# Optimization experiments

Hardware: AMD Instinct MI355X
Metric: run time of the kernel (lower is better)

## Reference

```python
import jax, jax.numpy as jnp
import numpy as np

D = 512      # model_size
NH = 8       # num_heads
HD = D // NH # head_dim = 64
T = 2048     # seq len (qlen == klen == pos len)
B = 2        # batch

# flattened Bayesian parameter layout (matches flatten_list order in the module)
_SHAPES = [(3 * D, D), (D, D), (D, D), (3 * D,), (D,), (D,), (NH, HD), (NH, HD)]
_N = sum(int(np.prod(s)) for s in _SHAPES)  # 1,314,304


def _unflatten(w):
    out, i = [], 0
    for s in _SHAPES:
        n = int(np.prod(s))
        out.append(w[i:i + n].reshape(s))
        i += n
    return out


def _rel_shift(x):
    # Transformer-XL relative shift: x is [qlen, klen, B, NH]
    q, k, b, n = x.shape
    x = jnp.pad(x, ((0, 0), (1, 0), (0, 0), (0, 0)))  # zero col at front of klen axis
    x = x.reshape(k + 1, q, b, n)[1:]
    return x.reshape(q, k, b, n)


def setup_inputs() -> dict:
    key = jax.random.key(0)
    k1, k2, k3, k4, k5 = jax.random.split(key, 5)
    inp = jax.random.normal(k1, (T, B, D), dtype=jnp.float32)
    pos = jax.random.normal(k2, (T, 1, D), dtype=jnp.float32)
    std = np.sqrt(2.0 / (D + D))
    mu = jax.random.normal(k3, (_N,), dtype=jnp.float32) * std
    rho = -5.0 + 0.1 * jax.random.normal(k4, (_N,), dtype=jnp.float32)
    eps = jax.random.normal(k5, (_N,), dtype=jnp.float32)
    attn_mask = jnp.triu(jnp.ones((T, T), dtype=bool), 1)  # True = masked (future)
    return {"input": inp, "pos": pos, "attn_mask": attn_mask,
            "mu": mu, "rho": rho, "eps": eps}


def reference(input, pos, attn_mask, mu, rho, eps):
    # Gaussian reparameterized weight sample: w = mu + softplus(rho) * eps
    w = mu + jax.nn.softplus(rho) * eps
    (in_w, out_w, pos_w, in_b, out_b, pos_b, r_w_bias, r_r_bias) = _unflatten(w)

    # input projection -> q, k, v : [T, B, NH, HD]
    qkv = input @ in_w.T + in_b                      # [T, B, 3D]
    q, k, v = jnp.split(qkv, 3, axis=-1)
    q = q.reshape(T, B, NH, HD)
    k = k.reshape(T, B, NH, HD)
    v = v.reshape(T, B, NH, HD)

    # relative position projection: [R, NH, HD]
    r = (pos[:, 0, :] @ pos_w.T + pos_b).reshape(-1, NH, HD)

    # content score (AC) and position score (BD) with rel-shift
    AC = jnp.einsum('ibnd,jbnd->ijbn', q + r_w_bias, k)
    BD = _rel_shift(jnp.einsum('ibnd,jnd->ijbn', q + r_r_bias, r))

    scale = np.float32(1.0 / np.sqrt(HD))
    score = (AC + BD) * scale                        # [T, T, B, NH]
    score = jnp.where(attn_mask[:, :, None, None],
                      jnp.finfo(score.dtype).min, score)
    probs = jax.nn.softmax(score, axis=1)

    attn_vec = jnp.einsum('ijbn,jbnd->ibnd', probs, v).reshape(T, B, D)
    return attn_vec @ out_w.T + out_b                # [T, B, D]
```

## Files before the change

kernel.cpp:

```cpp
#include <hip/hip_runtime.h>


typedef float f32x4 __attribute__((ext_vector_type(4)));
typedef short bf16x8 __attribute__((ext_vector_type(8)));

#define NW 1314304
#define OFF_INB  1310720
#define OFF_INW  0
#define OFF_OUTW 786432
#define OFF_POSW 1048576
#define BB_IN  0
#define BB_OUT 1536
#define BB_POS 2048
#define BB_RW  2560
#define BB_RR  3072

#define L2E 1.44269504088896340736f

__device__ __forceinline__ unsigned short f2bf(float x) {
  unsigned u = __builtin_bit_cast(unsigned, x);
  u += 0x7fffu + ((u >> 16) & 1u);
  return (unsigned short)(u >> 16);
}
__device__ __forceinline__ unsigned pk2(float lo, float hi) {
  return (unsigned)f2bf(lo) | ((unsigned)f2bf(hi) << 16);
}

__global__ void prep_kernel(const float* __restrict__ mu, const float* __restrict__ rho,
                            const float* __restrict__ eps,
                            const float* __restrict__ input, const float* __restrict__ pos,
                            unsigned short* __restrict__ Wh, float* __restrict__ Bf,
                            unsigned short* __restrict__ inH, unsigned short* __restrict__ posH) {
  const int bx = blockIdx.x;
  if (bx < 1284) {
    int i = (bx * 256 + threadIdx.x) * 4;
    if (i < NW) {
      float4 m = *(const float4*)&mu[i];
      float4 r = *(const float4*)&rho[i];
      float4 e = *(const float4*)&eps[i];
      float w0 = m.x + ((r.x > 20.f) ? r.x : log1pf(expf(r.x))) * e.x;
      float w1 = m.y + ((r.y > 20.f) ? r.y : log1pf(expf(r.y))) * e.y;
      float w2 = m.z + ((r.z > 20.f) ? r.z : log1pf(expf(r.z))) * e.z;
      float w3 = m.w + ((r.w > 20.f) ? r.w : log1pf(expf(r.w))) * e.w;
      union { unsigned short s[4]; uint2 u; } p;
      p.s[0] = f2bf(w0); p.s[1] = f2bf(w1); p.s[2] = f2bf(w2); p.s[3] = f2bf(w3);
      *(uint2*)&Wh[i] = p.u;
      if (i >= OFF_INB) {
        float4 b; b.x = w0; b.y = w1; b.z = w2; b.w = w3;
        *(float4*)&Bf[i - OFF_INB] = b;
      }
    }
  } else if (bx < 3332) {
    int i = ((bx - 1284) * 256 + threadIdx.x) * 4;
    float4 v = *(const float4*)&input[i];
    union { unsigned short s[4]; uint2 u; } p;
    p.s[0] = f2bf(v.x); p.s[1] = f2bf(v.y); p.s[2] = f2bf(v.z); p.s[3] = f2bf(v.w);
    *(uint2*)&inH[i] = p.u;
  } else {
    int i = ((bx - 3332) * 256 + threadIdx.x) * 4;
    float4 v = *(const float4*)&pos[i];
    union { unsigned short s[4]; uint2 u; } p;
    p.s[0] = f2bf(v.x); p.s[1] = f2bf(v.y); p.s[2] = f2bf(v.z); p.s[3] = f2bf(v.w);
    *(uint2*)&posH[i] = p.u;
  }
}

__device__ __forceinline__ void gemm_loop(const unsigned short* __restrict__ A,
                                          const unsigned short* __restrict__ B,
                                          unsigned short* As, unsigned short* Bs,
                                          f32x4 (&acc)[4]) {
  const int tid = threadIdx.x;
  const int wv = tid >> 6, lane = tid & 63, g = lane >> 4, cc = lane & 15;
  const int row = tid >> 2, q4 = tid & 3;
  const unsigned short* Ap = A + (size_t)row * 512 + 16 * q4;
  const unsigned short* Bp = B + (size_t)row * 512 + 16 * q4;

  *(uint4*)&As[row * 72 + 16 * q4]     = *(const uint4*)Ap;
  *(uint4*)&As[row * 72 + 16 * q4 + 8] = *(const uint4*)(Ap + 8);
  *(uint4*)&Bs[row * 72 + 16 * q4]     = *(const uint4*)Bp;
  *(uint4*)&Bs[row * 72 + 16 * q4 + 8] = *(const uint4*)(Bp + 8);
  __syncthreads();

  for (int it = 0; it < 8; it++) {
    uint4 a0, a1, b0, b1;
    const bool pf = (it < 7);
    if (pf) {
      const unsigned short* An = Ap + 64 * (it + 1);
      const unsigned short* Bn = Bp + 64 * (it + 1);
      a0 = *(const uint4*)An; a1 = *(const uint4*)(An + 8);
      b0 = *(const uint4*)Bn; b1 = *(const uint4*)(Bn + 8);
    }
    __builtin_amdgcn_s_setprio(1);
#pragma unroll
    for (int ks = 0; ks < 2; ks++) {
      bf16x8 af = *(const bf16x8*)&As[(16 * wv + cc) * 72 + 32 * ks + 8 * g];
#pragma unroll
      for (int fn = 0; fn < 4; fn++) {
        bf16x8 bf = *(const bf16x8*)&Bs[(16 * fn + cc) * 72 + 32 * ks + 8 * g];
        acc[fn] = __builtin_amdgcn_mfma_f32_16x16x32_bf16(af, bf, acc[fn], 0, 0, 0);
      }
    }
    __builtin_amdgcn_s_setprio(0);
    __syncthreads();
    if (pf) {
      *(uint4*)&As[row * 72 + 16 * q4]     = a0;
      *(uint4*)&As[row * 72 + 16 * q4 + 8] = a1;
      *(uint4*)&Bs[row * 72 + 16 * q4]     = b0;
      *(uint4*)&Bs[row * 72 + 16 * q4 + 8] = b1;
    }
    __syncthreads();
  }
}

__global__ __launch_bounds__(256, 2)
void gemm01_kernel(const unsigned short* __restrict__ inH, const unsigned short* __restrict__ posH,
                   const unsigned short* __restrict__ Wh, const float* __restrict__ Bf,
                   unsigned short* __restrict__ qrw, unsigned short* __restrict__ qrr,
                   unsigned short* __restrict__ kbuf, unsigned short* __restrict__ vT,
                   unsigned short* __restrict__ rbuf) {
  __shared__ __align__(16) unsigned short As[64 * 72];
  __shared__ __align__(16) unsigned short Bs[64 * 72];
  const int bx = blockIdx.x;
  const int tid = threadIdx.x;
  const int wv = tid >> 6, lane = tid & 63, g = lane >> 4, cc = lane & 15;

  const bool isR = (bx >= 1536);
  int m0, n0;
  const unsigned short *A, *W;
  if (!isR) {
    m0 = (bx & 63) << 6; n0 = (bx >> 6) << 6;
    A = inH + (size_t)m0 * 512;  W = Wh + OFF_INW + (size_t)n0 * 512;
  } else {
    const int t = bx - 1536;
    m0 = (t & 31) << 6; n0 = (t >> 5) << 6;
    A = posH + (size_t)m0 * 512; W = Wh + OFF_POSW + (size_t)n0 * 512;
  }

  f32x4 acc[4];
#pragma unroll
  for (int i = 0; i < 4; i++) { acc[i][0] = 0.f; acc[i][1] = 0.f; acc[i][2] = 0.f; acc[i][3] = 0.f; }
  gemm_loop(A, W, As, Bs, acc);

#pragma unroll
  for (int fn = 0; fn < 4; fn++) {
    const int col = n0 + 16 * fn + cc;
#pragma unroll
    for (int r = 0; r < 4; r++) {
      const int mrow = m0 + 16 * wv + 4 * g + r;
      float v = acc[fn][r];
      if (!isR) {
        v += Bf[BB_IN + col];
        const int sec = col >> 9;
        const int d = col & 511;
        const int nh = d >> 6, hd = d & 63;
        const int t = mrow >> 1, bb = mrow & 1;
        const size_t bi = ((size_t)(bb * 8 + nh) * 2048 + t) * 64 + hd;
        if (sec == 0) {
          qrw[bi] = f2bf(v + Bf[BB_RW + d]);
          qrr[bi] = f2bf(v + Bf[BB_RR + d]);
        } else if (sec == 1) {
          kbuf[bi] = f2bf(v);
        } else {
          vT[((size_t)(bb * 8 + nh) * 64 + hd) * 2048 + t] = f2bf(v);
        }
      } else {
        v += Bf[BB_POS + col];
        rbuf[((size_t)(col >> 6) * 2048 + mrow) * 64 + (col & 63)] = f2bf(v);
      }
    }
  }
}

__global__ __launch_bounds__(256, 2)
void gemmO_kernel(const unsigned short* __restrict__ av, const unsigned short* __restrict__ W,
                  const float* __restrict__ Bf, float* __restrict__ outp) {
  __shared__ __align__(16) unsigned short As[64 * 72];
  __shared__ __align__(16) unsigned short Bs[64 * 72];
  const int bx = blockIdx.x;
  const int tid = threadIdx.x;
  const int wv = tid >> 6, lane = tid & 63, g = lane >> 4, cc = lane & 15;
  const int m0 = (bx & 63) << 6, n0 = (bx >> 6) << 6;

  f32x4 acc[4];
#pragma unroll
  for (int i = 0; i < 4; i++) { acc[i][0] = 0.f; acc[i][1] = 0.f; acc[i][2] = 0.f; acc[i][3] = 0.f; }
  gemm_loop(av + (size_t)m0 * 512, W + (size_t)n0 * 512, As, Bs, acc);

#pragma unroll
  for (int fn = 0; fn < 4; fn++) {
    const int col = n0 + 16 * fn + cc;
#pragma unroll
    for (int r = 0; r < 4; r++) {
      const int mrow = m0 + 16 * wv + 4 * g + r;
      outp[(size_t)mrow * 512 + col] = acc[fn][r] + Bf[BB_OUT + col];
    }
  }
}

__global__ __launch_bounds__(256, 2)
void attn_kernel(const unsigned short* __restrict__ qrw, const unsigned short* __restrict__ qrr,
                 const unsigned short* __restrict__ kb, const unsigned short* __restrict__ vt,
                 const unsigned short* __restrict__ rb, unsigned short* __restrict__ av)
{
  __shared__ __align__(16) unsigned short Ks[64 * 72];
  __shared__ __align__(16) unsigned short Vs[64 * 72];
  __shared__ __align__(16) unsigned short Rs[128 * 72];
  __shared__ __align__(16) float Gs[4 * 80 * 20];

  const int tid = threadIdx.x;
  const int wv = tid >> 6, lane = tid & 63, g = lane >> 4, cc = lane & 15;
  const int bx = (int)blockIdx.x;
  const int idx = bx & 255;
  const int qt = (bx >> 8) ? (idx >> 4) : (31 - (idx >> 4));
  const int bn = idx & 15;
  const int nh = bn & 7, bb = bn >> 3;
  const int i0 = qt * 64;
  const int i0g = i0 + wv * 16;
  const int w0base = 1984 - i0;

  const size_t qko = (size_t)bn * 2048 * 64;
  const size_t ro = (size_t)nh * 2048 * 64;

  bf16x8 qw[2], qr[2];
#pragma unroll
  for (int ks = 0; ks < 2; ks++) {
    qw[ks] = *(const bf16x8*)&qrw[qko + (size_t)(i0g + cc) * 64 + 32 * ks + 8 * g];
    qr[ks] = *(const bf16x8*)&qrr[qko + (size_t)(i0g + cc) * 64 + 32 * ks + 8 * g];
  }

  float m_run = -3.0e38f, l_run = 0.f;
  f32x4 o[4];
#pragma unroll
  for (int i = 0; i < 4; i++) { o[i][0] = 0.f; o[i][1] = 0.f; o[i][2] = 0.f; o[i][3] = 0.f; }

  const int srow = tid >> 2, sq = tid & 3;
  const int rrow = tid >> 1, rhalf = tid & 1;
  float* Gw = &Gs[wv * 1600];
  const int rbase = 48 - 16 * wv;

  {
    const unsigned short* kp = &kb[qko + (size_t)srow * 64 + 16 * sq];
    *(uint4*)&Ks[srow * 72 + 16 * sq]     = *(const uint4*)kp;
    *(uint4*)&Ks[srow * 72 + 16 * sq + 8] = *(const uint4*)(kp + 8);
    const unsigned short* vp = &vt[qko + (size_t)srow * 2048 + 16 * sq];
    *(uint4*)&Vs[srow * 72 + 16 * sq]     = *(const uint4*)vp;
    *(uint4*)&Vs[srow * 72 + 16 * sq + 8] = *(const uint4*)(vp + 8);
    const int u0 = w0base + rrow;
    const int uc0 = u0 > 2047 ? 2047 : u0;
    const unsigned short* rp = &rb[ro + (size_t)uc0 * 64 + 32 * rhalf];
    unsigned short* rd = &Rs[(u0 & 127) * 72 + 32 * rhalf];
    *(uint4*)rd        = *(const uint4*)rp;
    *(uint4*)(rd + 8)  = *(const uint4*)(rp + 8);
    *(uint4*)(rd + 16) = *(const uint4*)(rp + 16);
    *(uint4*)(rd + 24) = *(const uint4*)(rp + 24);
  }
  __syncthreads();

  for (int kt = 0; kt <= qt; kt++) {
    const int j0 = kt * 64;
    const int w0k = w0base + j0;
    const bool pf = (kt < qt);

    uint4 ka0, ka1, va0, va1, ra0, ra1;
    int rslot = 0;
    if (pf) {
      const unsigned short* kp = &kb[qko + (size_t)(j0 + 64 + srow) * 64 + 16 * sq];
      ka0 = *(const uint4*)kp; ka1 = *(const uint4*)(kp + 8);
      const unsigned short* vp = &vt[qko + (size_t)srow * 2048 + j0 + 64 + 16 * sq];
      va0 = *(const uint4*)vp; va1 = *(const uint4*)(vp + 8);
      const int unew = w0k + 128 + (tid >> 2);
      rslot = unew & 127;
      const int uc = unew > 2047 ? 2047 : unew;
      const unsigned short* rp = &rb[ro + (size_t)uc * 64 + 16 * sq];
      ra0 = *(const uint4*)rp; ra1 = *(const uint4*)(rp + 8);
    }

    f32x4 st[4];
#pragma unroll
    for (int i = 0; i < 4; i++) { st[i][0] = 0.f; st[i][1] = 0.f; st[i][2] = 0.f; st[i][3] = 0.f; }
    __builtin_amdgcn_s_setprio(1);
#pragma unroll
    for (int ks = 0; ks < 2; ks++) {
#pragma unroll
      for (int fm = 0; fm < 4; fm++) {
        bf16x8 ka = *(const bf16x8*)&Ks[(16 * fm + cc) * 72 + 32 * ks + 8 * g];
        st[fm] = __builtin_amdgcn_mfma_f32_16x16x32_bf16(ka, qw[ks], st[fm], 0, 0, 0);
      }
    }
    f32x4 gt[5];
#pragma unroll
    for (int i = 0; i < 5; i++) { gt[i][0] = 0.f; gt[i][1] = 0.f; gt[i][2] = 0.f; gt[i][3] = 0.f; }
    const int rr0 = w0k + rbase + cc;
#pragma unroll
    for (int ks = 0; ks < 2; ks++) {
#pragma unroll
      for (int fm = 0; fm < 5; fm++) {
        const int rrw = (rr0 + 16 * fm) & 127;
        bf16x8 ra = *(const bf16x8*)&Rs[rrw * 72 + 32 * ks + 8 * g];
        gt[fm] = __builtin_amdgcn_mfma_f32_16x16x32_bf16(ra, qr[ks], gt[fm], 0, 0, 0);
      }
    }
    __builtin_amdgcn_s_setprio(0);
#pragma unroll
    for (int fm = 0; fm < 5; fm++)
#pragma unroll
      for (int r = 0; r < 4; r++)
        Gw[(16 * fm + 4 * g + r) * 20 + cc] = gt[fm][r];

    float p[4][4];
    float tm = -3.0e38f;
    const bool diag = (kt == qt);
#pragma unroll
    for (int fm = 0; fm < 4; fm++) {
#pragma unroll
      for (int r = 0; r < 4; r++) {
        const int jj = 16 * fm + 4 * g + r;
        float bd = Gw[(jj - cc + 15) * 20 + cc];
        float sv = (st[fm][r] + bd) * 0.125f;
        if (diag && (jj > cc + 16 * wv)) sv = -3.0e38f;
        p[fm][r] = sv;
        tm = fmaxf(tm, sv);
      }
    }
    tm = fmaxf(tm, __shfl_xor(tm, 16));
    tm = fmaxf(tm, __shfl_xor(tm, 32));
    const float m_new = fmaxf(m_run, tm);
    const float sc = exp2f((m_run - m_new) * L2E);
    float ps = 0.f;
#pragma unroll
    for (int fm = 0; fm < 4; fm++)
#pragma unroll
      for (int r = 0; r < 4; r++) {
        float pv = exp2f((p[fm][r] - m_new) * L2E);
        p[fm][r] = pv;
        ps += pv;
      }
    ps += __shfl_xor(ps, 16);
    ps += __shfl_xor(ps, 32);
    l_run = l_run * sc + ps;
    m_run = m_new;

    float scr[4];
#pragma unroll
    for (int r = 0; r < 4; r++) scr[r] = __shfl(sc, 4 * g + r);
#pragma unroll
    for (int fn = 0; fn < 4; fn++)
#pragma unroll
      for (int r = 0; r < 4; r++) o[fn][r] *= scr[r];

    unsigned u01[4], u23[4];
#pragma unroll
    for (int fm = 0; fm < 4; fm++) {
      u01[fm] = pk2(p[fm][0], p[fm][1]);
      u23[fm] = pk2(p[fm][2], p[fm][3]);
    }
    bf16x8 pa[2];
#pragma unroll
    for (int ks = 0; ks < 2; ks++) {
      union { unsigned u[4]; bf16x8 v; } pw;
#pragma unroll
      for (int j = 0; j < 4; j++) {
        const int srcl = (2 * (g & 1) + (j >> 1)) * 16 + cc;
        unsigned v0 = __shfl((j & 1) ? u23[2 * ks] : u01[2 * ks], srcl);
        unsigned v1 = __shfl((j & 1) ? u23[2 * ks + 1] : u01[2 * ks + 1], srcl);
        pw.u[j] = (g >> 1) ? v1 : v0;
      }
      pa[ks] = pw.v;
    }
    __builtin_amdgcn_s_setprio(1);
#pragma unroll
    for (int ks = 0; ks < 2; ks++) {
#pragma unroll
      for (int fn = 0; fn < 4; fn++) {
        bf16x8 vb = *(const bf16x8*)&Vs[(16 * fn + cc) * 72 + 32 * ks + 8 * g];
        o[fn] = __builtin_amdgcn_mfma_f32_16x16x32_bf16(pa[ks], vb, o[fn], 0, 0, 0);
      }
    }
    __builtin_amdgcn_s_setprio(0);

    __syncthreads();
    if (pf) {
      *(uint4*)&Ks[srow * 72 + 16 * sq]     = ka0;
      *(uint4*)&Ks[srow * 72 + 16 * sq + 8] = ka1;
      *(uint4*)&Vs[srow * 72 + 16 * sq]     = va0;
      *(uint4*)&Vs[srow * 72 + 16 * sq + 8] = va1;
      unsigned short* rd = &Rs[rslot * 72 + 16 * sq];
      *(uint4*)rd       = ra0;
      *(uint4*)(rd + 8) = ra1;
    }
    __syncthreads();
  }

  const float inv = 1.0f / l_run;
  float invr[4];
#pragma unroll
  for (int r = 0; r < 4; r++) invr[r] = __shfl(inv, 4 * g + r);
#pragma unroll
  for (int fn = 0; fn < 4; fn++) {
    const int hd = 16 * fn + cc;
#pragma unroll
    for (int r = 0; r < 4; r++) {
      const int irow = i0g + 4 * g + r;
      av[((size_t)(irow * 2 + bb) * 8 + nh) * 64 + hd] = f2bf(o[fn][r] * invr[r]);
    }
  }
}

extern "C" void kernel_launch(void* const* d_in, const int* in_sizes, int n_in,
                              void* d_out, int out_size, void* d_ws, size_t ws_size,
                              hipStream_t stream) {
  const float* input = (const float*)d_in[0];
  const float* pos   = (const float*)d_in[1];
  const float* mu  = (const float*)d_in[3];
  const float* rho = (const float*)d_in[4];
  const float* eps = (const float*)d_in[5];
  float* out = (float*)d_out;

  char* ws = (char*)d_ws;
  unsigned short* Wh   = (unsigned short*)ws;
  float*          Bf   = (float*)(ws + 2628608);
  unsigned short* inH  = (unsigned short*)(ws + 2642944);
  unsigned short* posH = (unsigned short*)(ws + 6837248);
  unsigned short* qrw  = (unsigned short*)(ws + 8934400);
  unsigned short* qrr  = (unsigned short*)(ws + 13128704);
  unsigned short* kbuf = (unsigned short*)(ws + 17323008);
  unsigned short* vT   = (unsigned short*)(ws + 21517312);
  unsigned short* rbuf = (unsigned short*)(ws + 25711616);
  unsigned short* av   = inH;

  prep_kernel<<<dim3(4356), dim3(256), 0, stream>>>(mu, rho, eps, input, pos, Wh, Bf, inH, posH);
  gemm01_kernel<<<dim3(1792), dim3(256), 0, stream>>>(inH, posH, Wh, Bf, qrw, qrr, kbuf, vT, rbuf);
  attn_kernel<<<dim3(512), dim3(256), 0, stream>>>(qrw, qrr, kbuf, vT, rbuf, av);
  gemmO_kernel<<<dim3(512), dim3(256), 0, stream>>>(av, Wh + OFF_OUTW, Bf, out);
}
```

Baseline: 173.9 us.

## Split causal attention over key chunks with a combine pass; coalesce vT stores

The attention kernel now splits each query tile's key range into chunks of up to 8 key tiles, giving 1280 roughly balanced blocks instead of 512 with uneven causal work. Partial outputs and softmax stats are written to a workspace and merged by a new combine kernel. Separately, the V-section of the QKV GEMM transposes through shared memory so vT is written with 16-byte coalesced stores. The BD scratch buffer is stored as bf16 to cut LDS, and occupancy is raised to 3 blocks per SIMD, at the cost of an extra launch, partial-output traffic and some precision loss.

```diff
diff --git a/kernel.cpp b/kernel.cpp
--- a/kernel.cpp
+++ b/kernel.cpp
@@ -21,6 +21,9 @@
   unsigned u = __builtin_bit_cast(unsigned, x);
   u += 0x7fffu + ((u >> 16) & 1u);
   return (unsigned short)(u >> 16);
+}
+__device__ __forceinline__ float bf2f(unsigned short s) {
+  return __builtin_bit_cast(float, ((unsigned)s) << 16);
 }
 __device__ __forceinline__ unsigned pk2(float lo, float hi) {
   return (unsigned)f2bf(lo) | ((unsigned)f2bf(hi) << 16);
@@ -141,6 +144,30 @@
   for (int i = 0; i < 4; i++) { acc[i][0] = 0.f; acc[i][1] = 0.f; acc[i][2] = 0.f; acc[i][3] = 0.f; }
   gemm_loop(A, W, As, Bs, acc);
 
+  const int sec = n0 >> 9;
+  if (!isR && sec == 2) {
+#pragma unroll
+    for (int fn = 0; fn < 4; fn++) {
+      const int col = n0 + 16 * fn + cc;
+#pragma unroll
+      for (int r = 0; r < 4; r++)
+        As[(16 * wv + 4 * g + r) * 72 + 16 * fn + cc] = f2bf(acc[fn][r] + Bf[BB_IN + col]);
+    }
+    __syncthreads();
+    const int nh2 = (n0 >> 6) & 7;
+#pragma unroll
+    for (int cpass = 0; cpass < 2; cpass++) {
+      const int ch = tid + cpass * 256;
+      const int ncol = ch >> 3, bb2 = (ch >> 2) & 1, jc = ch & 3;
+      union { unsigned short s[8]; uint4 u; } pk;
+#pragma unroll
+      for (int jj = 0; jj < 8; jj++)
+        pk.s[jj] = As[(2 * (8 * jc + jj) + bb2) * 72 + ncol];
+      *(uint4*)&vT[((size_t)(bb2 * 8 + nh2) * 64 + ncol) * 2048 + (m0 >> 1) + 8 * jc] = pk.u;
+    }
+    return;
+  }
+
 #pragma unroll
   for (int fn = 0; fn < 4; fn++) {
     const int col = n0 + 16 * fn + cc;
@@ -150,7 +177,6 @@
       float v = acc[fn][r];
       if (!isR) {
         v += Bf[BB_IN + col];
-        const int sec = col >> 9;
         const int d = col & 511;
         const int nh = d >> 6, hd = d & 63;
         const int t = mrow >> 1, bb = mrow & 1;
@@ -158,10 +184,8 @@
         if (sec == 0) {
           qrw[bi] = f2bf(v + Bf[BB_RW + d]);
           qrr[bi] = f2bf(v + Bf[BB_RR + d]);
-        } else if (sec == 1) {
+        } else {
           kbuf[bi] = f2bf(v);
-        } else {
-          vT[((size_t)(bb * 8 + nh) * 64 + hd) * 2048 + t] = f2bf(v);
         }
       } else {
         v += Bf[BB_POS + col];
@@ -197,22 +221,30 @@
   }
 }
 
-__global__ __launch_bounds__(256, 2)
+__global__ __launch_bounds__(256, 3)
 void attn_kernel(const unsigned short* __restrict__ qrw, const unsigned short* __restrict__ qrr,
                  const unsigned short* __restrict__ kb, const unsigned short* __restrict__ vt,
-                 const unsigned short* __restrict__ rb, unsigned short* __restrict__ av)
+                 const unsigned short* __restrict__ rb, unsigned short* __restrict__ av,
+                 unsigned short* __restrict__ pO, float* __restrict__ pStats)
 {
   __shared__ __align__(16) unsigned short Ks[64 * 72];
   __shared__ __align__(16) unsigned short Vs[64 * 72];
   __shared__ __align__(16) unsigned short Rs[128 * 72];
-  __shared__ __align__(16) float Gs[4 * 80 * 20];
+  __shared__ __align__(16) unsigned short Gs[4 * 80 * 20];
 
   const int tid = threadIdx.x;
   const int wv = tid >> 6, lane = tid & 63, g = lane >> 4, cc = lane & 15;
   const int bx = (int)blockIdx.x;
-  const int idx = bx & 255;
-  const int qt = (bx >> 8) ? (idx >> 4) : (31 - (idx >> 4));
-  const int bn = idx & 15;
+  const int bn = bx & 15;
+  const int sid = 79 - (bx >> 4);
+  int qt, s, ns;
+  if (sid < 8)       { qt = sid;                s = 0;           ns = 1; }
+  else if (sid < 24) { qt = 8 + ((sid - 8) >> 1); s = (sid - 8) & 1; ns = 2; }
+  else if (sid < 48) { const int t = sid - 24; const int q3 = t / 3; qt = 16 + q3; s = t - 3 * q3; ns = 3; }
+  else               { const int t = sid - 48; qt = 24 + (t >> 2); s = t & 3; ns = 4; }
+  const int kt0 = s * 8;
+  const int kt1 = (kt0 + 8 < qt + 1) ? (kt0 + 8) : (qt + 1);
+
   const int nh = bn & 7, bb = bn >> 3;
   const int i0 = qt * 64;
   const int i0g = i0 + wv * 16;
@@ -235,17 +267,17 @@
 
   const int srow = tid >> 2, sq = tid & 3;
   const int rrow = tid >> 1, rhalf = tid & 1;
-  float* Gw = &Gs[wv * 1600];
+  unsigned short* Gw = &Gs[wv * 1600];
   const int rbase = 48 - 16 * wv;
 
   {
-    const unsigned short* kp = &kb[qko + (size_t)srow * 64 + 16 * sq];
+    const unsigned short* kp = &kb[qko + (size_t)(kt0 * 64 + srow) * 64 + 16 * sq];
     *(uint4*)&Ks[srow * 72 + 16 * sq]     = *(const uint4*)kp;
     *(uint4*)&Ks[srow * 72 + 16 * sq + 8] = *(const uint4*)(kp + 8);
-    const unsigned short* vp = &vt[qko + (size_t)srow * 2048 + 16 * sq];
+    const unsigned short* vp = &vt[qko + (size_t)srow * 2048 + kt0 * 64 + 16 * sq];
     *(uint4*)&Vs[srow * 72 + 16 * sq]     = *(const uint4*)vp;
     *(uint4*)&Vs[srow * 72 + 16 * sq + 8] = *(const uint4*)(vp + 8);
-    const int u0 = w0base + rrow;
+    const int u0 = w0base + kt0 * 64 + rrow;
     const int uc0 = u0 > 2047 ? 2047 : u0;
     const unsigned short* rp = &rb[ro + (size_t)uc0 * 64 + 32 * rhalf];
     unsigned short* rd = &Rs[(u0 & 127) * 72 + 32 * rhalf];
@@ -256,10 +288,10 @@
   }
   __syncthreads();
 
-  for (int kt = 0; kt <= qt; kt++) {
+  for (int kt = kt0; kt < kt1; kt++) {
     const int j0 = kt * 64;
     const int w0k = w0base + j0;
-    const bool pf = (kt < qt);
+    const bool pf = (kt + 1 < kt1);
 
     uint4 ka0, ka1, va0, va1, ra0, ra1;
     int rslot = 0;
@@ -305,7 +337,7 @@
     for (int fm = 0; fm < 5; fm++)
 #pragma unroll
       for (int r = 0; r < 4; r++)
-        Gw[(16 * fm + 4 * g + r) * 20 + cc] = gt[fm][r];
+        Gw[(16 * fm + 4 * g + r) * 20 + cc] = f2bf(gt[fm][r]);
 
     float p[4][4];
     float tm = -3.0e38f;
@@ -315,7 +347,7 @@
 #pragma unroll
       for (int r = 0; r < 4; r++) {
         const int jj = 16 * fm + 4 * g + r;
-        float bd = Gw[(jj - cc + 15) * 20 + cc];
+        float bd = bf2f(Gw[(jj - cc + 15) * 20 + cc]);
         float sv = (st[fm][r] + bd) * 0.125f;
         if (diag && (jj > cc + 16 * wv)) sv = -3.0e38f;
         p[fm][r] = sv;
@@ -391,19 +423,82 @@
     __syncthreads();
   }
 
-  const float inv = 1.0f / l_run;
-  float invr[4];
-#pragma unroll
-  for (int r = 0; r < 4; r++) invr[r] = __shfl(inv, 4 * g + r);
-#pragma unroll
-  for (int fn = 0; fn < 4; fn++) {
-    const int hd = 16 * fn + cc;
-#pragma unroll
-    for (int r = 0; r < 4; r++) {
-      const int irow = i0g + 4 * g + r;
-      av[((size_t)(irow * 2 + bb) * 8 + nh) * 64 + hd] = f2bf(o[fn][r] * invr[r]);
-    }
-  }
+  if (ns == 1) {
+    const float inv = 1.0f / l_run;
+    float invr[4];
+#pragma unroll
+    for (int r = 0; r < 4; r++) invr[r] = __shfl(inv, 4 * g + r);
+#pragma unroll
+    for (int fn = 0; fn < 4; fn++) {
+      const int hd = 16 * fn + cc;
+#pragma unroll
+      for (int r = 0; r < 4; r++) {
+        const int irow = i0g + 4 * g + r;
+        av[((size_t)(irow * 2 + bb) * 8 + nh) * 64 + hd] = f2bf(o[fn][r] * invr[r]);
+      }
+    }
+  } else {
+    const size_t slot = (size_t)(bn * 80 + sid);
+#pragma unroll
+    for (int fn = 0; fn < 4; fn++) {
+      const int hd = 16 * fn + cc;
+#pragma unroll
+      for (int r = 0; r < 4; r++)
+        pO[slot * 4096 + (16 * wv + 4 * g + r) * 64 + hd] = f2bf(o[fn][r]);
+    }
+    if (g == 0) {
+      pStats[slot * 128 + (16 * wv + cc) * 2]     = m_run;
+      pStats[slot * 128 + (16 * wv + cc) * 2 + 1] = l_run;
+    }
+  }
+}
+
+__global__ __launch_bounds__(256)
+void combine_kernel(const unsigned short* __restrict__ pO, const float* __restrict__ pStats,
+                    unsigned short* __restrict__ av) {
+  const int bxx = (int)blockIdx.x;
+  const int bn = bxx & 15, qt = 8 + (bxx >> 4);
+  const int nh = bn & 7, bb = bn >> 3;
+  const int ns = (qt >> 3) + 1;
+  const int sid0 = (qt < 16) ? (8 + (qt - 8) * 2)
+                 : (qt < 24) ? (24 + (qt - 16) * 3)
+                             : (48 + (qt - 24) * 4);
+  const int tid = threadIdx.x;
+  const int ql = tid >> 2, hq = tid & 3;
+  const size_t sb = (size_t)(bn * 80 + sid0);
+
+  float M = -3.0e38f;
+  for (int i = 0; i < ns; i++)
+    M = fmaxf(M, pStats[(sb + i) * 128 + ql * 2]);
+
+  float L = 0.f;
+  float accv[16];
+#pragma unroll
+  for (int j = 0; j < 16; j++) accv[j] = 0.f;
+  for (int i = 0; i < ns; i++) {
+    const float mi = pStats[(sb + i) * 128 + ql * 2];
+    const float li = pStats[(sb + i) * 128 + ql * 2 + 1];
+    const float w = exp2f((mi - M) * L2E);
+    L += w * li;
+    union { uint4 u; unsigned short s[8]; } c0, c1;
+    const unsigned short* src = &pO[(sb + i) * 4096 + ql * 64 + 16 * hq];
+    c0.u = *(const uint4*)src;
+    c1.u = *(const uint4*)(src + 8);
+#pragma unroll
+    for (int j = 0; j < 8; j++) accv[j]     += w * bf2f(c0.s[j]);
+#pragma unroll
+    for (int j = 0; j < 8; j++) accv[8 + j] += w * bf2f(c1.s[j]);
+  }
+  const float inv = 1.0f / L;
+  union { uint4 u; unsigned short s[8]; } o0, o1;
+#pragma unroll
+  for (int j = 0; j < 8; j++) o0.s[j] = f2bf(accv[j] * inv);
+#pragma unroll
+  for (int j = 0; j < 8; j++) o1.s[j] = f2bf(accv[8 + j] * inv);
+  const int q = qt * 64 + ql;
+  unsigned short* dst = &av[((size_t)(q * 2 + bb) * 8 + nh) * 64 + 16 * hq];
+  *(uint4*)dst       = o0.u;
+  *(uint4*)(dst + 8) = o1.u;
 }
 
 extern "C" void kernel_launch(void* const* d_in, const int* in_sizes, int n_in,
@@ -426,10 +521,13 @@
   unsigned short* kbuf = (unsigned short*)(ws + 17323008);
   unsigned short* vT   = (unsigned short*)(ws + 21517312);
   unsigned short* rbuf = (unsigned short*)(ws + 25711616);
+  unsigned short* pO   = (unsigned short*)(ws + 27808768);
+  float*          pSt  = (float*)(ws + 38294528);
   unsigned short* av   = inH;
 
   prep_kernel<<<dim3(4356), dim3(256), 0, stream>>>(mu, rho, eps, input, pos, Wh, Bf, inH, posH);
   gemm01_kernel<<<dim3(1792), dim3(256), 0, stream>>>(inH, posH, Wh, Bf, qrw, qrr, kbuf, vT, rbuf);
-  attn_kernel<<<dim3(512), dim3(256), 0, stream>>>(qrw, qrr, kbuf, vT, rbuf, av);
+  attn_kernel<<<dim3(1280), dim3(256), 0, stream>>>(qrw, qrr, kbuf, vT, rbuf, av, pO, pSt);
+  combine_kernel<<<dim3(384), dim3(256), 0, stream>>>(pO, pSt, av);
   gemmO_kernel<<<dim3(512), dim3(256), 0, stream>>>(av, Wh + OFF_OUTW, Bf, out);
 }
```

Measured after the change: 174.6 us. No clear change (+0.4%).
